# Kernel tuning notes

Hardware: AMD Instinct MI355X
Metric: run time of the kernel (lower is better)

The kernel has to match this reference:

```python
import jax, jax.numpy as jnp
import numpy as np

N_NODES = 50000
N_EDGES = 800000
IN_CH, HID, LAT = 256, 128, 64


def setup_inputs() -> dict:
    key = jax.random.key(0)
    k1, k2, k3, k4 = jax.random.split(key, 4)
    x = jax.random.normal(k1, (N_NODES, IN_CH), dtype=jnp.float32)
    edge_index = jax.random.randint(k2, (2, N_EDGES), 0, N_NODES, dtype=jnp.int64)
    W1 = jax.random.normal(k3, (IN_CH, HID), dtype=jnp.float32) * (1.0 / np.sqrt(IN_CH))
    b1 = jnp.zeros((HID,), dtype=jnp.float32)
    W2 = jax.random.normal(k4, (HID, LAT), dtype=jnp.float32) * (1.0 / np.sqrt(HID))
    b2 = jnp.zeros((LAT,), dtype=jnp.float32)
    return {"x": x, "edge_index": edge_index, "W1": W1, "b1": b1, "W2": W2, "b2": b2}


def gcn_conv(x, src, dst, deg_inv_sqrt, W, b):
    # PyG GCNConv: h = x @ W; out[dst] += d_dst^-1/2 * d_src^-1/2 * h[src]; + bias
    h = x @ W                                   # [N, out]
    norm = deg_inv_sqrt[src] * deg_inv_sqrt[dst]  # [E+N]
    msg = h[src] * norm[:, None]                # [E+N, out] (gather + scale)
    out = jax.ops.segment_sum(msg, dst, num_segments=x.shape[0])
    return out + b


def reference(x, edge_index, W1, b1, W2, b2):
    n = x.shape[0]
    loop = jnp.arange(n, dtype=edge_index.dtype)
    # add self loops (GCNConv default)
    src = jnp.concatenate([edge_index[0], loop])
    dst = jnp.concatenate([edge_index[1], loop])
    deg = jax.ops.segment_sum(jnp.ones_like(dst, dtype=x.dtype), dst, num_segments=n)
    deg_inv_sqrt = jnp.where(deg > 0, jax.lax.rsqrt(deg), 0.0)
    h = jax.nn.relu(gcn_conv(x, src, dst, deg_inv_sqrt, W1, b1))
    h = jax.nn.relu(gcn_conv(h, src, dst, deg_inv_sqrt, W2, b2))
    return h
```

## Files before the change

### kernel.cpp

```cpp
#include <hip/hip_runtime.h>

#define N_NODES 50000
#define N_EDGES 800000
#define IN_CH 256
#define HID 128
#define LAT 64
#define CAP 64
#define NBIN 196
#define BINCAP 4864

typedef __attribute__((ext_vector_type(8))) short short8;
typedef __attribute__((ext_vector_type(16))) float f32x16;

static __device__ __forceinline__ unsigned short bf16_rne(float x) {
    unsigned u = __float_as_uint(x);
    unsigned r = (u + 0x7FFFu + ((u >> 16) & 1u)) >> 16;
    return (unsigned short)r;
}
static __device__ __forceinline__ float bf16_to_f(unsigned short h) {
    return __uint_as_float(((unsigned)h) << 16);
}

static __device__ __forceinline__ void add8(uint4 p, float* a) {
    a[0] += __uint_as_float(p.x << 16);
    a[1] += __uint_as_float(p.x & 0xFFFF0000u);
    a[2] += __uint_as_float(p.y << 16);
    a[3] += __uint_as_float(p.y & 0xFFFF0000u);
    a[4] += __uint_as_float(p.z << 16);
    a[5] += __uint_as_float(p.z & 0xFFFF0000u);
    a[6] += __uint_as_float(p.w << 16);
    a[7] += __uint_as_float(p.w & 0xFFFF0000u);
}
static __device__ __forceinline__ void fma8(uint4 p, float m, float* a) {
    a[0] = fmaf(m, __uint_as_float(p.x << 16), a[0]);
    a[1] = fmaf(m, __uint_as_float(p.x & 0xFFFF0000u), a[1]);
    a[2] = fmaf(m, __uint_as_float(p.y << 16), a[2]);
    a[3] = fmaf(m, __uint_as_float(p.y & 0xFFFF0000u), a[3]);
    a[4] = fmaf(m, __uint_as_float(p.z << 16), a[4]);
    a[5] = fmaf(m, __uint_as_float(p.z & 0xFFFF0000u), a[5]);
    a[6] = fmaf(m, __uint_as_float(p.w << 16), a[6]);
    a[7] = fmaf(m, __uint_as_float(p.w & 0xFFFF0000u), a[7]);
}

template <int K, int NN>
static __device__ __forceinline__ void split_store(const float* __restrict__ W,
                                                   unsigned short* __restrict__ Wf, int i) {
    constexpr int CT = NN / 32;
    int k = i / NN, n = i % NN;
    float w = W[i];
    unsigned short hi = bf16_rne(w);
    unsigned short lo = bf16_rne(w - bf16_to_f(hi));
    size_t off = ((size_t)((k >> 4) * CT + (n >> 5)) * 64 + ((n & 31) + 32 * ((k >> 3) & 1))) * 8 + (k & 7);
    Wf[off] = hi;
    Wf[(size_t)K * NN + off] = lo;
}

__global__ __launch_bounds__(256) void prep_kernel(const float* __restrict__ W1,
                                                   const float* __restrict__ W2,
                                                   int* __restrict__ binCnt,
                                                   unsigned short* __restrict__ W1f,
                                                   unsigned short* __restrict__ W2f) {
    int i = blockIdx.x * blockDim.x + threadIdx.x;
    if (i < NBIN) binCnt[i] = 0;
    if (i < IN_CH * HID) split_store<IN_CH, HID>(W1, W1f, i);
    if (i < HID * LAT) split_store<HID, LAT>(W2, W2f, i);
}

__global__ __launch_bounds__(256) void fill1_kernel(const int* __restrict__ ei,
                                                    int* __restrict__ binCnt,
                                                    unsigned int* __restrict__ binBuf, int E) {
    __shared__ int hist[NBIN];
    __shared__ int base[NBIN];
    const int tid = threadIdx.x;
    for (int i = tid; i < NBIN; i += 256) hist[i] = 0;
    __syncthreads();

    const int e0 = blockIdx.x * 2048 + tid;
    unsigned int pk[8];
    int bn[8], ofs[8];
#pragma unroll
    for (int i = 0; i < 8; ++i) {
        int e = e0 + 256 * i;
        bool v = e < E;
        int s = v ? ei[e] : 0;
        int d = v ? ei[E + e] : 0;
        bn[i] = d >> 8;
        pk[i] = (unsigned int)s | ((unsigned int)(d & 255) << 16);
        ofs[i] = v ? atomicAdd(&hist[bn[i]], 1) : -1;
    }
    __syncthreads();
    for (int i = tid; i < NBIN; i += 256)
        base[i] = hist[i] ? atomicAdd(&binCnt[i], hist[i]) : 0;
    __syncthreads();
#pragma unroll
    for (int i = 0; i < 8; ++i) {
        if (ofs[i] >= 0) {
            int p = base[bn[i]] + ofs[i];
            if (p < BINCAP) binBuf[(size_t)bn[i] * BINCAP + p] = pk[i];
        }
    }
}

__global__ __launch_bounds__(256) void fill2_kernel(const int* __restrict__ binCnt,
                                                    const unsigned int* __restrict__ binBuf,
                                                    int* __restrict__ cnt,
                                                    unsigned short* __restrict__ colb) {
    __shared__ int lcnt[256];
    const int b = blockIdx.x;
    const int tid = threadIdx.x;
    lcnt[tid] = 0;
    __syncthreads();
    int n = binCnt[b]; if (n > BINCAP) n = BINCAP;
    const int node0 = b << 8;
    for (int i = tid; i < n; i += 256) {
        unsigned int pk = binBuf[(size_t)b * BINCAP + i];
        int local = pk >> 16;
        int s = pk & 0xFFFF;
        int slot = atomicAdd(&lcnt[local], 1);
        if (slot < CAP) colb[(size_t)(node0 + local) * CAP + slot] = (unsigned short)s;
    }
    __syncthreads();
    int node = node0 + tid;
    if (node < N_NODES) cnt[node] = lcnt[tid];
}

template <int K, int NN, bool AFP32>
__global__ __launch_bounds__(256) void gemm_kernel(const void* __restrict__ Av,
                                                   const unsigned short* __restrict__ Wf,
                                                   const int* __restrict__ cnt,
                                                   unsigned short* __restrict__ C, int M) {
    constexpr int CT = NN / 32;
    constexpr int NT = (NN == 128) ? 2 : 1;
    __shared__ unsigned short As[4 * 512];
    __shared__ unsigned short Bs[2 * 2 * CT * 512];

    const int tid = threadIdx.x;
    const int lane = tid & 63;
    const int w = tid >> 6;
    const int row0 = blockIdx.x * 64;
    const int rt = w >> 1;
    const int ct0 = (NN == 128) ? ((w & 1) * 2) : (w & 1);

    f32x16 acc[NT];
#pragma unroll
    for (int nt = 0; nt < NT; ++nt)
#pragma unroll
        for (int q = 0; q < 16; ++q) acc[nt][q] = 0.0f;

    for (int kt = 0; kt < K; kt += 32) {
        {
            int m = tid >> 2, kc = tid & 3;
            int row = row0 + m; if (row >= M) row = M - 1;
            int s = kc >> 1, half = kc & 1, t = m >> 5;
            int ln = (m & 31) + 32 * half;
            uint4 v;
            if constexpr (AFP32) {
                const float* A = (const float*)Av;
                const float4 v0 = *(const float4*)(A + (size_t)row * K + kt + kc * 8);
                const float4 v1 = *(const float4*)(A + (size_t)row * K + kt + kc * 8 + 4);
                v.x = (unsigned)bf16_rne(v0.x) | ((unsigned)bf16_rne(v0.y) << 16);
                v.y = (unsigned)bf16_rne(v0.z) | ((unsigned)bf16_rne(v0.w) << 16);
                v.z = (unsigned)bf16_rne(v1.x) | ((unsigned)bf16_rne(v1.y) << 16);
                v.w = (unsigned)bf16_rne(v1.z) | ((unsigned)bf16_rne(v1.w) << 16);
            } else {
                const unsigned short* A = (const unsigned short*)Av;
                v = *(const uint4*)(A + (size_t)row * K + kt + kc * 8);
            }
            *(uint4*)&As[((s * 2 + t) << 9) + (ln << 3)] = v;
        }
        {
            const int sg0 = kt >> 4;
#pragma unroll
            for (int i0 = 0; i0 < CT * 256; i0 += 256) {
                int i = i0 + tid;
                int psl = i / (CT * 64), rem = i % (CT * 64);
                int p = psl >> 1, sl = psl & 1;
                const uint4* src = (const uint4*)(Wf + (size_t)p * K * NN + (size_t)(sg0 + sl) * CT * 512);
                ((uint4*)Bs)[i] = src[rem];
            }
        }
        __syncthreads();

#pragma unroll
        for (int sl = 0; sl < 2; ++sl) {
            short8 a = *(const short8*)&As[((sl * 2 + rt) << 9) + (lane << 3)];
            short8 bh[NT], bl[NT];
#pragma unroll
            for (int nt = 0; nt < NT; ++nt) {
                bh[nt] = *(const short8*)&Bs[((sl * CT + ct0 + nt) << 9) + (lane << 3)];
                bl[nt] = *(const short8*)&Bs[(((2 + sl) * CT + ct0 + nt) << 9) + (lane << 3)];
            }
#pragma unroll
            for (int nt = 0; nt < NT; ++nt) {
                acc[nt] = __builtin_amdgcn_mfma_f32_32x32x16_bf16(a, bh[nt], acc[nt], 0, 0, 0);
                acc[nt] = __builtin_amdgcn_mfma_f32_32x32x16_bf16(a, bl[nt], acc[nt], 0, 0, 0);
            }
        }
        __syncthreads();
    }

#pragma unroll
    for (int r = 0; r < 16; ++r) {
        int rowl = rt * 32 + (r & 3) + 8 * (r >> 2) + 4 * (lane >> 5);
        int row = row0 + rowl;
        if (row < M) {
            float sc = rsqrtf((float)cnt[row] + 1.0f);
#pragma unroll
            for (int nt = 0; nt < NT; ++nt) {
                int col = (ct0 + nt) * 32 + (lane & 31);
                C[(size_t)row * NN + col] = bf16_rne(acc[nt][r] * sc);
            }
        }
    }
}

template <int C, bool OBF16>
__global__ __launch_bounds__(256) void agg_kernel(const int* __restrict__ cnt,
                                                  const unsigned short* __restrict__ colb,
                                                  const unsigned short* __restrict__ hs,
                                                  const float* __restrict__ bias,
                                                  void* __restrict__ outv, int N) {
    constexpr int LPN = C / 8;
    constexpr int NPW = 64 / LPN;
    int node = (int)((blockIdx.x * blockDim.x + threadIdx.x) >> 6);
    int lane = threadIdx.x & 63;
    if (node >= N) return;
    const int g = lane / LPN;
    const int c = lane % LPN;

    int deg = cnt[node];
    int kk = deg < CAP ? deg : CAP;

    float acc[8];
#pragma unroll
    for (int q = 0; q < 8; ++q) acc[q] = 0.0f;
    if (g == 0) add8(*(const uint4*)(hs + (size_t)node * C + c * 8), acc);

    int myc = (lane < kk) ? (int)colb[(size_t)node * CAP + lane] : 0;

    int j = 0;
    for (; j + NPW * 4 <= kk; j += NPW * 4) {
        int s0 = __shfl(myc, j + g);
        int s1 = __shfl(myc, j + g + NPW);
        int s2 = __shfl(myc, j + g + 2 * NPW);
        int s3 = __shfl(myc, j + g + 3 * NPW);
        uint4 p0 = *(const uint4*)(hs + (size_t)s0 * C + c * 8);
        uint4 p1 = *(const uint4*)(hs + (size_t)s1 * C + c * 8);
        uint4 p2 = *(const uint4*)(hs + (size_t)s2 * C + c * 8);
        uint4 p3 = *(const uint4*)(hs + (size_t)s3 * C + c * 8);
        add8(p0, acc); add8(p1, acc); add8(p2, acc); add8(p3, acc);
    }
    if (j < kk) {
        bool v0 = (j + g) < kk, v1 = (j + g + NPW) < kk,
             v2 = (j + g + 2 * NPW) < kk, v3 = (j + g + 3 * NPW) < kk;
        int s0 = __shfl(myc, v0 ? (j + g) : 0);
        int s1 = __shfl(myc, v1 ? (j + g + NPW) : 0);
        int s2 = __shfl(myc, v2 ? (j + g + 2 * NPW) : 0);
        int s3 = __shfl(myc, v3 ? (j + g + 3 * NPW) : 0);
        uint4 p0 = *(const uint4*)(hs + (size_t)s0 * C + c * 8);
        uint4 p1 = *(const uint4*)(hs + (size_t)s1 * C + c * 8);
        uint4 p2 = *(const uint4*)(hs + (size_t)s2 * C + c * 8);
        uint4 p3 = *(const uint4*)(hs + (size_t)s3 * C + c * 8);
        fma8(p0, v0 ? 1.0f : 0.0f, acc);
        fma8(p1, v1 ? 1.0f : 0.0f, acc);
        fma8(p2, v2 ? 1.0f : 0.0f, acc);
        fma8(p3, v3 ? 1.0f : 0.0f, acc);
    }

#pragma unroll
    for (int s = LPN; s < 64; s <<= 1)
#pragma unroll
        for (int q = 0; q < 8; ++q) acc[q] += __shfl_xor(acc[q], s);

    if (lane < LPN) {
        float di = rsqrtf((float)deg + 1.0f);
        float o[8];
#pragma unroll
        for (int q = 0; q < 8; ++q)
            o[q] = fmaxf(fmaf(di, acc[q], bias[c * 8 + q]), 0.0f);
        if constexpr (OBF16) {
            unsigned short* out = (unsigned short*)outv;
            ushort4 lo4 = make_ushort4(bf16_rne(o[0]), bf16_rne(o[1]), bf16_rne(o[2]), bf16_rne(o[3]));
            ushort4 hi4 = make_ushort4(bf16_rne(o[4]), bf16_rne(o[5]), bf16_rne(o[6]), bf16_rne(o[7]));
            *(ushort4*)(out + (size_t)node * C + c * 8) = lo4;
            *(ushort4*)(out + (size_t)node * C + c * 8 + 4) = hi4;
        } else {
            float* out = (float*)outv;
            float4 o0 = {o[0], o[1], o[2], o[3]};
            float4 o1 = {o[4], o[5], o[6], o[7]};
            *(float4*)(out + (size_t)node * C + c * 8) = o0;
            *(float4*)(out + (size_t)node * C + c * 8 + 4) = o1;
        }
    }
}

extern "C" void kernel_launch(void* const* d_in, const int* in_sizes, int n_in,
                              void* d_out, int out_size, void* d_ws, size_t ws_size,
                              hipStream_t stream) {
    const float* x  = (const float*)d_in[0];
    const int*   ei = (const int*)d_in[1];
    const float* W1 = (const float*)d_in[2];
    const float* b1 = (const float*)d_in[3];
    const float* W2 = (const float*)d_in[4];
    const float* b2 = (const float*)d_in[5];

    const int N = N_NODES, E = N_EDGES;

    char* ws = (char*)d_ws;
    size_t off = 0;
    auto alloc = [&](size_t bytes) {
        void* p = ws + off;
        off = (off + bytes + 255) & ~(size_t)255;
        return p;
    };
    int*            cnt    = (int*)alloc((size_t)N * 4);
    unsigned short* colb   = (unsigned short*)alloc((size_t)N * CAP * 2);
    int*            binCnt = (int*)alloc((size_t)NBIN * 4);
    unsigned int*   binBuf = (unsigned int*)alloc((size_t)NBIN * BINCAP * 4);
    unsigned short* W1f    = (unsigned short*)alloc((size_t)2 * IN_CH * HID * 2);
    unsigned short* W2f    = (unsigned short*)alloc((size_t)2 * HID * LAT * 2);
    unsigned short* h1s    = (unsigned short*)alloc((size_t)N * HID * 2);
    unsigned short* act1   = (unsigned short*)alloc((size_t)N * HID * 2);
    unsigned short* h2s    = h1s;

    prep_kernel<<<(N + 255) / 256, 256, 0, stream>>>(W1, W2, binCnt, W1f, W2f);
    fill1_kernel<<<(E + 2047) / 2048, 256, 0, stream>>>(ei, binCnt, binBuf, E);
    fill2_kernel<<<NBIN, 256, 0, stream>>>(binCnt, binBuf, cnt, colb);

    gemm_kernel<IN_CH, HID, true><<<(N + 63) / 64, 256, 0, stream>>>(x, W1f, cnt, h1s, N);
    agg_kernel<HID, true><<<(N + 3) / 4, 256, 0, stream>>>(cnt, colb, h1s, b1, act1, N);

    gemm_kernel<HID, LAT, false><<<(N + 63) / 64, 256, 0, stream>>>(act1, W2f, cnt, h2s, N);
    agg_kernel<LAT, false><<<(N + 3) / 4, 256, 0, stream>>>(cnt, colb, h2s, b2, d_out, N);
}
```

Before: 198.3 us.

## Fuse all GCN stages into one cooperative persistent kernel with grid syncs

Merges the seven separate launches (weight prep, two binning passes, two GEMMs, two aggregations) into a single cooperative kernel of 512 blocks. The stages are separated by grid.sync() and share one LDS union, while GEMM tiles and aggregation groups are distributed with grid-stride loops. The aim is to remove per-launch overhead and inter-kernel gaps. In exchange it caps residency at two blocks per CU, which limits latency hiding for the gather-heavy aggregation. It also adds six grid-wide barriers and leaves GEMM tiles split unevenly across blocks (782 tiles over 512 blocks).

```diff
diff --git a/kernel.cpp b/kernel.cpp
--- a/kernel.cpp
+++ b/kernel.cpp
@@ -1,4 +1,7 @@
 #include <hip/hip_runtime.h>
+#include <hip/hip_cooperative_groups.h>
+
+namespace cg = cooperative_groups;
 
 #define N_NODES 50000
 #define N_EDGES 800000
@@ -8,6 +11,10 @@
 #define CAP 64
 #define NBIN 196
 #define BINCAP 4864
+#define GRID 512
+#define NCHUNK ((N_EDGES + 2047) / 2048)
+#define NTILE ((N_NODES + 63) / 64)
+#define NGRP ((N_NODES + 3) / 4)
 
 typedef __attribute__((ext_vector_type(8))) short short8;
 typedef __attribute__((ext_vector_type(16))) float f32x16;
@@ -55,60 +62,51 @@
     Wf[(size_t)K * NN + off] = lo;
 }
 
-__global__ __launch_bounds__(256) void prep_kernel(const float* __restrict__ W1,
-                                                   const float* __restrict__ W2,
+union SharedU {
+    struct { int hist[NBIN]; int base[NBIN]; } f1;
+    int lcnt[256];
+    struct { unsigned short As[2048]; unsigned short Bs[8192]; } g;
+};
+
+static __device__ __forceinline__ void fill1_block(const int* __restrict__ ei,
                                                    int* __restrict__ binCnt,
-                                                   unsigned short* __restrict__ W1f,
-                                                   unsigned short* __restrict__ W2f) {
-    int i = blockIdx.x * blockDim.x + threadIdx.x;
-    if (i < NBIN) binCnt[i] = 0;
-    if (i < IN_CH * HID) split_store<IN_CH, HID>(W1, W1f, i);
-    if (i < HID * LAT) split_store<HID, LAT>(W2, W2f, i);
-}
-
-__global__ __launch_bounds__(256) void fill1_kernel(const int* __restrict__ ei,
-                                                    int* __restrict__ binCnt,
-                                                    unsigned int* __restrict__ binBuf, int E) {
-    __shared__ int hist[NBIN];
-    __shared__ int base[NBIN];
-    const int tid = threadIdx.x;
-    for (int i = tid; i < NBIN; i += 256) hist[i] = 0;
-    __syncthreads();
-
-    const int e0 = blockIdx.x * 2048 + tid;
+                                                   unsigned int* __restrict__ binBuf,
+                                                   int c, int tid, SharedU& sm) {
+    for (int i = tid; i < NBIN; i += 256) sm.f1.hist[i] = 0;
+    __syncthreads();
+
+    const int e0 = c * 2048 + tid;
     unsigned int pk[8];
     int bn[8], ofs[8];
 #pragma unroll
     for (int i = 0; i < 8; ++i) {
         int e = e0 + 256 * i;
-        bool v = e < E;
+        bool v = e < N_EDGES;
         int s = v ? ei[e] : 0;
-        int d = v ? ei[E + e] : 0;
+        int d = v ? ei[N_EDGES + e] : 0;
         bn[i] = d >> 8;
         pk[i] = (unsigned int)s | ((unsigned int)(d & 255) << 16);
-        ofs[i] = v ? atomicAdd(&hist[bn[i]], 1) : -1;
+        ofs[i] = v ? atomicAdd(&sm.f1.hist[bn[i]], 1) : -1;
     }
     __syncthreads();
     for (int i = tid; i < NBIN; i += 256)
-        base[i] = hist[i] ? atomicAdd(&binCnt[i], hist[i]) : 0;
+        sm.f1.base[i] = sm.f1.hist[i] ? atomicAdd(&binCnt[i], sm.f1.hist[i]) : 0;
     __syncthreads();
 #pragma unroll
     for (int i = 0; i < 8; ++i) {
         if (ofs[i] >= 0) {
-            int p = base[bn[i]] + ofs[i];
+            int p = sm.f1.base[bn[i]] + ofs[i];
             if (p < BINCAP) binBuf[(size_t)bn[i] * BINCAP + p] = pk[i];
         }
     }
 }
 
-__global__ __launch_bounds__(256) void fill2_kernel(const int* __restrict__ binCnt,
-                                                    const unsigned int* __restrict__ binBuf,
-                                                    int* __restrict__ cnt,
-                                                    unsigned short* __restrict__ colb) {
-    __shared__ int lcnt[256];
-    const int b = blockIdx.x;
-    const int tid = threadIdx.x;
-    lcnt[tid] = 0;
+static __device__ __forceinline__ void fill2_block(const int* __restrict__ binCnt,
+                                                   const unsigned int* __restrict__ binBuf,
+                                                   int* __restrict__ cnt,
+                                                   unsigned short* __restrict__ colb,
+                                                   int b, int tid, SharedU& sm) {
+    sm.lcnt[tid] = 0;
     __syncthreads();
     int n = binCnt[b]; if (n > BINCAP) n = BINCAP;
     const int node0 = b << 8;
@@ -116,28 +114,28 @@
         unsigned int pk = binBuf[(size_t)b * BINCAP + i];
         int local = pk >> 16;
         int s = pk & 0xFFFF;
-        int slot = atomicAdd(&lcnt[local], 1);
+        int slot = atomicAdd(&sm.lcnt[local], 1);
         if (slot < CAP) colb[(size_t)(node0 + local) * CAP + slot] = (unsigned short)s;
     }
     __syncthreads();
     int node = node0 + tid;
-    if (node < N_NODES) cnt[node] = lcnt[tid];
+    if (node < N_NODES) cnt[node] = sm.lcnt[tid];
 }
 
 template <int K, int NN, bool AFP32>
-__global__ __launch_bounds__(256) void gemm_kernel(const void* __restrict__ Av,
-                                                   const unsigned short* __restrict__ Wf,
-                                                   const int* __restrict__ cnt,
-                                                   unsigned short* __restrict__ C, int M) {
+static __device__ __forceinline__ void gemm_tile(const void* __restrict__ Av,
+                                                 const unsigned short* __restrict__ Wf,
+                                                 const int* __restrict__ cnt,
+                                                 unsigned short* __restrict__ C,
+                                                 int tile, int tid, SharedU& sm) {
     constexpr int CT = NN / 32;
     constexpr int NT = (NN == 128) ? 2 : 1;
-    __shared__ unsigned short As[4 * 512];
-    __shared__ unsigned short Bs[2 * 2 * CT * 512];
-
-    const int tid = threadIdx.x;
+    unsigned short* As = sm.g.As;
+    unsigned short* Bs = sm.g.Bs;
+    const int M = N_NODES;
     const int lane = tid & 63;
     const int w = tid >> 6;
-    const int row0 = blockIdx.x * 64;
+    const int row0 = tile * 64;
     const int rt = w >> 1;
     const int ct0 = (NN == 128) ? ((w & 1) * 2) : (w & 1);
 
@@ -215,16 +213,17 @@
 }
 
 template <int C, bool OBF16>
-__global__ __launch_bounds__(256) void agg_kernel(const int* __restrict__ cnt,
-                                                  const unsigned short* __restrict__ colb,
-                                                  const unsigned short* __restrict__ hs,
-                                                  const float* __restrict__ bias,
-                                                  void* __restrict__ outv, int N) {
+static __device__ __forceinline__ void agg_group(const int* __restrict__ cnt,
+                                                 const unsigned short* __restrict__ colb,
+                                                 const unsigned short* __restrict__ hs,
+                                                 const float* __restrict__ bias,
+                                                 void* __restrict__ outv,
+                                                 int grp, int tid) {
     constexpr int LPN = C / 8;
     constexpr int NPW = 64 / LPN;
-    int node = (int)((blockIdx.x * blockDim.x + threadIdx.x) >> 6);
-    int lane = threadIdx.x & 63;
-    if (node >= N) return;
+    int node = grp * 4 + (tid >> 6);
+    int lane = tid & 63;
+    if (node >= N_NODES) return;
     const int g = lane / LPN;
     const int c = lane % LPN;
 
@@ -294,6 +293,41 @@
     }
 }
 
+__global__ void __launch_bounds__(256, 2) fused_kernel(
+    const float* x, const int* ei, const float* W1, const float* b1,
+    const float* W2, const float* b2, float* out,
+    int* cnt, unsigned short* colb, int* binCnt, unsigned int* binBuf,
+    unsigned short* W1f, unsigned short* W2f,
+    unsigned short* h1s, unsigned short* act1) {
+    __shared__ SharedU sm;
+    cg::grid_group grid = cg::this_grid();
+    const int tid = threadIdx.x;
+    const int bid = blockIdx.x;
+
+    {
+        int i = bid * 256 + tid;
+        if (i < NBIN) binCnt[i] = 0;
+        if (i < IN_CH * HID) split_store<IN_CH, HID>(W1, W1f, i);
+        if (i < HID * LAT) split_store<HID, LAT>(W2, W2f, i);
+    }
+    grid.sync();
+    if (bid < NCHUNK) fill1_block(ei, binCnt, binBuf, bid, tid, sm);
+    grid.sync();
+    if (bid < NBIN) fill2_block(binCnt, binBuf, cnt, colb, bid, tid, sm);
+    grid.sync();
+    for (int t = bid; t < NTILE; t += GRID)
+        gemm_tile<IN_CH, HID, true>(x, W1f, cnt, h1s, t, tid, sm);
+    grid.sync();
+    for (int g = bid; g < NGRP; g += GRID)
+        agg_group<HID, true>(cnt, colb, h1s, b1, act1, g, tid);
+    grid.sync();
+    for (int t = bid; t < NTILE; t += GRID)
+        gemm_tile<HID, LAT, false>(act1, W2f, cnt, h1s, t, tid, sm);
+    grid.sync();
+    for (int g = bid; g < NGRP; g += GRID)
+        agg_group<LAT, false>(cnt, colb, h1s, b2, out, g, tid);
+}
+
 extern "C" void kernel_launch(void* const* d_in, const int* in_sizes, int n_in,
                               void* d_out, int out_size, void* d_ws, size_t ws_size,
                               hipStream_t stream) {
@@ -303,8 +337,7 @@
     const float* b1 = (const float*)d_in[3];
     const float* W2 = (const float*)d_in[4];
     const float* b2 = (const float*)d_in[5];
-
-    const int N = N_NODES, E = N_EDGES;
+    float* out = (float*)d_out;
 
     char* ws = (char*)d_ws;
     size_t off = 0;
@@ -313,23 +346,19 @@
         off = (off + bytes + 255) & ~(size_t)255;
         return p;
     };
-    int*            cnt    = (int*)alloc((size_t)N * 4);
-    unsigned short* colb   = (unsigned short*)alloc((size_t)N * CAP * 2);
+    int*            cnt    = (int*)alloc((size_t)N_NODES * 4);
+    unsigned short* colb   = (unsigned short*)alloc((size_t)N_NODES * CAP * 2);
     int*            binCnt = (int*)alloc((size_t)NBIN * 4);
     unsigned int*   binBuf = (unsigned int*)alloc((size_t)NBIN * BINCAP * 4);
     unsigned short* W1f    = (unsigned short*)alloc((size_t)2 * IN_CH * HID * 2);
     unsigned short* W2f    = (unsigned short*)alloc((size_t)2 * HID * LAT * 2);
-    unsigned short* h1s    = (unsigned short*)alloc((size_t)N * HID * 2);
-    unsigned short* act1   = (unsigned short*)alloc((size_t)N * HID * 2);
-    unsigned short* h2s    = h1s;
-
-    prep_kernel<<<(N + 255) / 256, 256, 0, stream>>>(W1, W2, binCnt, W1f, W2f);
-    fill1_kernel<<<(E + 2047) / 2048, 256, 0, stream>>>(ei, binCnt, binBuf, E);
-    fill2_kernel<<<NBIN, 256, 0, stream>>>(binCnt, binBuf, cnt, colb);
-
-    gemm_kernel<IN_CH, HID, true><<<(N + 63) / 64, 256, 0, stream>>>(x, W1f, cnt, h1s, N);
-    agg_kernel<HID, true><<<(N + 3) / 4, 256, 0, stream>>>(cnt, colb, h1s, b1, act1, N);
-
-    gemm_kernel<HID, LAT, false><<<(N + 63) / 64, 256, 0, stream>>>(act1, W2f, cnt, h2s, N);
-    agg_kernel<LAT, false><<<(N + 3) / 4, 256, 0, stream>>>(cnt, colb, h2s, b2, d_out, N);
-}
+    unsigned short* h1s    = (unsigned short*)alloc((size_t)N_NODES * HID * 2);
+    unsigned short* act1   = (unsigned short*)alloc((size_t)N_NODES * HID * 2);
+
+    void* args[] = {(void*)&x, (void*)&ei, (void*)&W1, (void*)&b1,
+                    (void*)&W2, (void*)&b2, (void*)&out,
+                    (void*)&cnt, (void*)&colb, (void*)&binCnt, (void*)&binBuf,
+                    (void*)&W1f, (void*)&W2f, (void*)&h1s, (void*)&act1};
+    hipLaunchCooperativeKernel((const void*)fused_kernel, dim3(GRID), dim3(256),
+                               args, 0, stream);
+}
```

New measurement: 594.9 us. 3x slower.
